# Optimization experiments

Hardware: AMD Instinct MI355X
Metric: run time of the kernel (lower is better)

Reference implementation:

```python
import jax, jax.numpy as jnp
import numpy as np

N_HEAD = 12
N_EMBD = 768


def setup_inputs() -> dict:
    key = jax.random.key(0)
    ks = jax.random.split(key, 5)
    B, T, C = 8, 1024, N_EMBD
    x = jax.random.normal(ks[0], (B, T, C), dtype=jnp.float32)
    # c_attn: Linear(C, 3C); c_proj: Linear(C, C). PyTorch Linear: y = x @ W.T + b
    s = 1.0 / np.sqrt(C)
    W_attn = jax.random.uniform(ks[1], (3 * C, C), minval=-s, maxval=s, dtype=jnp.float32)
    b_attn = jax.random.uniform(ks[2], (3 * C,), minval=-s, maxval=s, dtype=jnp.float32)
    W_proj = jax.random.uniform(ks[3], (C, C), minval=-s, maxval=s, dtype=jnp.float32)
    b_proj = jax.random.uniform(ks[4], (C,), minval=-s, maxval=s, dtype=jnp.float32)
    return {"x": x, "W_attn": W_attn, "b_attn": b_attn, "W_proj": W_proj, "b_proj": b_proj}


def reference(x, W_attn, b_attn, W_proj, b_proj):
    B, T, C = x.shape
    H = N_HEAD
    hs = C // H  # head size
    qkv = x @ W_attn.T + b_attn  # [B, T, 3C]
    q, k, v = jnp.split(qkv, 3, axis=2)
    # [B, T, H, hs] -> [B, H, T, hs]
    q = q.reshape(B, T, H, hs).transpose(0, 2, 1, 3)
    k = k.reshape(B, T, H, hs).transpose(0, 2, 1, 3)
    v = v.reshape(B, T, H, hs).transpose(0, 2, 1, 3)
    att = jnp.einsum('bhqd,bhkd->bhqk', q, k) * (1.0 / np.sqrt(hs))
    causal = jnp.tril(jnp.ones((T, T), dtype=bool))
    att = jnp.where(causal, att, -jnp.inf)
    att = jax.nn.softmax(att, axis=-1)
    y = jnp.einsum('bhqk,bhkd->bhqd', att, v)  # [B, H, T, hs]
    y = y.transpose(0, 2, 1, 3).reshape(B, T, C)
    return y @ W_proj.T + b_proj
```

## Files before the change

### kernel.cpp

```cpp
#include <hip/hip_runtime.h>

typedef unsigned short u16;
typedef unsigned int u32;
typedef __attribute__((ext_vector_type(8))) __bf16 bf16x8;
typedef __attribute__((ext_vector_type(4))) float f32x4;
typedef __attribute__((ext_vector_type(4))) int i32x4;

#define MFMA16(a, b, c) __builtin_amdgcn_mfma_f32_16x16x32_bf16(a, b, c, 0, 0, 0)

__device__ __forceinline__ u16 f2b(float f) {
  __bf16 h = (__bf16)f;
  return __builtin_bit_cast(u16, h);
}

__device__ __forceinline__ void gl_lds16(const void* g, void* l) {
  __builtin_amdgcn_global_load_lds(
      (const __attribute__((address_space(1))) void*)g,
      (__attribute__((address_space(3))) void*)l, 16, 0, 0);
}

__device__ __forceinline__ bf16x8 ldf(const void* p) {
  return __builtin_bit_cast(bf16x8, *(const i32x4*)p);
}

__global__ __launch_bounds__(256) void cvt3_kernel(
    const float4* __restrict__ a, ushort4* __restrict__ oa, int na4,
    const float4* __restrict__ b, ushort4* __restrict__ ob, int nb4,
    const float4* __restrict__ c, ushort4* __restrict__ oc, int nc4) {
  const int step = gridDim.x * blockDim.x;
  const int t0 = blockIdx.x * blockDim.x + threadIdx.x;
  for (int i = t0; i < na4; i += step) {
    float4 v = a[i];
    ushort4 o; o.x = f2b(v.x); o.y = f2b(v.y); o.z = f2b(v.z); o.w = f2b(v.w);
    oa[i] = o;
  }
  for (int i = t0; i < nb4; i += step) {
    float4 v = b[i];
    ushort4 o; o.x = f2b(v.x); o.y = f2b(v.y); o.z = f2b(v.z); o.w = f2b(v.w);
    ob[i] = o;
  }
  for (int i = t0; i < nc4; i += step) {
    float4 v = c[i];
    ushort4 o; o.x = f2b(v.x); o.y = f2b(v.y); o.z = f2b(v.z); o.w = f2b(v.w);
    oc[i] = o;
  }
}

template <int BM, int EPI>
__global__ __launch_bounds__(256, 3) void gemm4(
    const u16* __restrict__ A, const u16* __restrict__ B,
    const float* __restrict__ bias, int M, int N, int K,
    u16* __restrict__ q_s, u16* __restrict__ k_s, u16* __restrict__ vt_s,
    float* __restrict__ outf) {
  constexpr int BN = 192;
  constexpr int MR = BM / 32;
  constexpr int NR = 6;
  constexpr int IA = BM / 32;
  constexpr int IB = 6;
  __shared__ __align__(16) u16 As[BM * 64];
  __shared__ __align__(16) u16 Bs[BN * 64];
  const int tid = threadIdx.x;
  const int w = tid >> 6, l = tid & 63;
  const int lo = l & 15, hi = l >> 4;
  const int wr = w >> 1, wc = w & 1;
  const int nwg = gridDim.x * gridDim.y;
  int bid = blockIdx.y * gridDim.x + blockIdx.x;
  bid = (bid & 7) * (nwg >> 3) + (bid >> 3);
  const int bm0 = (bid / gridDim.x) * BM;
  const int bn0 = (bid % gridDim.x) * BN;
  const size_t Kb = (size_t)K * 2;
  const char* Ab = (const char*)A;
  const char* Bb = (const char*)B;
  const int lrow8 = l >> 3;
  const int lcol = (l & 7) * 16;

  f32x4 acc[MR][NR] = {};

  for (int kt = 0; kt < K; kt += 64) {
    __syncthreads();
#pragma unroll
    for (int i = 0; i < IA; ++i) {
      int rl = (w * IA + i) * 8 + lrow8;
      int cb = lcol ^ ((rl & 7) << 4);
      gl_lds16(Ab + (size_t)(bm0 + rl) * Kb + kt * 2 + cb,
               (char*)As + (w * IA + i) * 1024);
    }
#pragma unroll
    for (int i = 0; i < IB; ++i) {
      int rl = (w * IB + i) * 8 + lrow8;
      int cb = lcol ^ ((rl & 7) << 4);
      gl_lds16(Bb + (size_t)(bn0 + rl) * Kb + kt * 2 + cb,
               (char*)Bs + (w * IB + i) * 1024);
    }
    __syncthreads();
#pragma unroll
    for (int ks = 0; ks < 2; ++ks) {
      bf16x8 bfr[NR];
#pragma unroll
      for (int nf = 0; nf < NR; ++nf) {
        int r = wc * 96 + nf * 16 + lo;
        bfr[nf] = ldf((char*)Bs + r * 128 + ((ks * 64 + hi * 16) ^ ((r & 7) << 4)));
      }
#pragma unroll
      for (int mf = 0; mf < MR; ++mf) {
        int r = wr * (MR * 16) + mf * 16 + lo;
        bf16x8 afr = ldf((char*)As + r * 128 + ((ks * 64 + hi * 16) ^ ((r & 7) << 4)));
#pragma unroll
        for (int nf = 0; nf < NR; ++nf) acc[mf][nf] = MFMA16(afr, bfr[nf], acc[mf][nf]);
      }
    }
  }

#pragma unroll
  for (int nf = 0; nf < NR; ++nf) {
    int col = bn0 + wc * 96 + nf * 16 + lo;
    float bv = bias[col];
    if (EPI == 0) {
      int seg = col / 768;
      int cs = col - seg * 768;
      int h = cs >> 6, d = cs & 63;
      u16* dst = (seg == 0) ? q_s : k_s;
#pragma unroll
      for (int mf = 0; mf < MR; ++mf) {
        int m0 = bm0 + wr * (MR * 16) + mf * 16 + hi * 4;
        int bb = m0 >> 10, t0 = m0 & 1023;
        size_t bh = (size_t)(bb * 12 + h);
        if (seg < 2) {
#pragma unroll
          for (int r = 0; r < 4; ++r)
            dst[(bh * 1024 + t0 + r) * 64 + d] = f2b(acc[mf][nf][r] + bv);
        } else {
          ushort4 pk;
          pk.x = f2b(acc[mf][nf][0] + bv);
          pk.y = f2b(acc[mf][nf][1] + bv);
          pk.z = f2b(acc[mf][nf][2] + bv);
          pk.w = f2b(acc[mf][nf][3] + bv);
          *(ushort4*)&vt_s[(bh * 64 + d) * 1024 + t0] = pk;
        }
      }
    } else {
#pragma unroll
      for (int mf = 0; mf < MR; ++mf) {
        int m0 = bm0 + wr * (MR * 16) + mf * 16 + hi * 4;
#pragma unroll
        for (int r = 0; r < 4; ++r) outf[(size_t)(m0 + r) * N + col] = acc[mf][nf][r] + bv;
      }
    }
  }
}

__global__ __launch_bounds__(256) void attn_kernel(
    const u16* __restrict__ Q, const u16* __restrict__ Kg,
    const u16* __restrict__ Vt, u16* __restrict__ Y) {
  __shared__ __align__(16) u16 Ks[3][64 * 64];
  __shared__ __align__(16) u16 Vs[3][64 * 64];
  const int tid = threadIdx.x;
  const int w = tid >> 6, l = tid & 63;
  const int lo = l & 15, hi = l >> 4;
  int bid = blockIdx.y * gridDim.x + blockIdx.x;
  bid = (bid & 7) * 96 + (bid >> 3);
  const int bh = bid >> 3;
  const int pr = bid & 7;
  const int b = bh / 12, h = bh % 12;
  const float c1 = 0.125f * 1.44269504f;
  const int swl = (lo & 7) << 4;
  const u16* Qb = Q + (size_t)bh * 65536;
  const char* Kbp = (const char*)(Kg + (size_t)bh * 65536);
  const char* Vbp = (const char*)(Vt + (size_t)bh * 65536);
  const int shbase = lo + ((l & 16) ? 32 : 0);
  const bool hiLow = (l & 32) == 0;

  bf16x8 onesv;
#pragma unroll
  for (int j = 0; j < 8; ++j) onesv[j] = (__bf16)1.0f;

  auto STAGE = [&](int buf, int kb) {
#pragma unroll
    for (int i = 0; i < 2; ++i) {
      int c = w * 2 + i;
      int row = c * 8 + (l >> 3);
      int cb = ((l & 7) * 16) ^ ((row & 7) << 4);
      gl_lds16(Kbp + (size_t)(kb + row) * 128 + cb, (char*)&Ks[buf][0] + c * 1024);
      gl_lds16(Vbp + (size_t)row * 2048 + (size_t)kb * 2 + cb, (char*)&Vs[buf][0] + c * 1024);
    }
  };

  for (int sg = 0; sg < 2; ++sg) {
    const int tile = sg ? (15 - pr) : pr;
    const int q0 = tile * 64 + w * 16;
    const int nt = tile + 1;
    const int qr = q0 + lo;

    bf16x8 qf[2];
#pragma unroll
    for (int ks = 0; ks < 2; ++ks)
      qf[ks] = ldf(Qb + (size_t)(q0 + lo) * 64 + ks * 32 + hi * 8);

    f32x4 o[4] = {};
    f32x4 lsum = {0.f, 0.f, 0.f, 0.f};
    float mrow = -1e30f;

    __builtin_amdgcn_s_barrier();
    STAGE(0, 0);
    if (nt > 1) STAGE(1, 64);

    for (int kt = 0; kt < nt; ++kt) {
      if (kt + 1 < nt)
        asm volatile("s_waitcnt vmcnt(4)" ::: "memory");
      else
        asm volatile("s_waitcnt vmcnt(0)" ::: "memory");
      __builtin_amdgcn_s_barrier();
      __builtin_amdgcn_sched_barrier(0);
      if (kt + 2 < nt) STAGE((kt + 2) % 3, (kt + 2) * 64);
      const char* Kt = (const char*)&Ks[kt % 3][0];
      const char* Vv = (const char*)&Vs[kt % 3][0];
      const int kb = kt * 64;

      f32x4 st[4] = {};
      __builtin_amdgcn_s_setprio(1);
#pragma unroll
      for (int kf = 0; kf < 4; ++kf) {
        int rb = (kf * 16 + lo) * 128;
#pragma unroll
        for (int ks = 0; ks < 2; ++ks)
          st[kf] = MFMA16(ldf(Kt + rb + ((ks * 64 + hi * 16) ^ swl)), qf[ks], st[kf]);
      }
      __builtin_amdgcn_s_setprio(0);
      bf16x8 vb[4][2];
#pragma unroll
      for (int nd = 0; nd < 4; ++nd) {
        int rb = (nd * 16 + lo) * 128;
#pragma unroll
        for (int ks = 0; ks < 2; ++ks)
          vb[nd][ks] = ldf(Vv + rb + ((ks * 64 + hi * 16) ^ swl));
      }
      if (kt == nt - 1) {
#pragma unroll
        for (int kf = 0; kf < 4; ++kf)
#pragma unroll
          for (int r = 0; r < 4; ++r) {
            int kcol = kb + kf * 16 + hi * 4 + r;
            if (kcol > qr) st[kf][r] = -1e30f;
          }
      }
      float lm = st[0][0];
#pragma unroll
      for (int kf = 0; kf < 4; ++kf)
#pragma unroll
        for (int r = 0; r < 4; ++r) lm = fmaxf(lm, st[kf][r]);
      lm = fmaxf(lm, __shfl_xor(lm, 16));
      lm = fmaxf(lm, __shfl_xor(lm, 32));
      if (__any(lm * c1 > mrow + 8.0f)) {
        float Mn = fmaxf(mrow, lm * c1);
        float alP = __builtin_amdgcn_exp2f(mrow - Mn);
        mrow = Mn;
        f32x4 alo;
#pragma unroll
        for (int r = 0; r < 4; ++r) alo[r] = __shfl(alP, hi * 4 + r);
#pragma unroll
        for (int nd = 0; nd < 4; ++nd)
#pragma unroll
          for (int r = 0; r < 4; ++r) o[nd][r] *= alo[r];
#pragma unroll
        for (int r = 0; r < 4; ++r) lsum[r] *= alo[r];
      }
#pragma unroll
      for (int kf = 0; kf < 4; ++kf)
#pragma unroll
        for (int r = 0; r < 4; ++r)
          st[kf][r] = __builtin_amdgcn_exp2f(fmaf(st[kf][r], c1, -mrow));
      u32 pk[4][2];
#pragma unroll
      for (int kf = 0; kf < 4; ++kf)
#pragma unroll
        for (int rp = 0; rp < 2; ++rp)
          pk[kf][rp] = (u32)f2b(st[kf][2 * rp]) | ((u32)f2b(st[kf][2 * rp + 1]) << 16);
      bf16x8 pa[2];
#pragma unroll
      for (int ks = 0; ks < 2; ++ks) {
        i32x4 wv;
#pragma unroll
        for (int s = 0; s < 4; ++s) {
          int src = shbase + ((s >> 1) << 4);
          u32 xa = __shfl(pk[2 * ks][s & 1], src);
          u32 xb = __shfl(pk[2 * ks + 1][s & 1], src);
          wv[s] = (int)(hiLow ? xa : xb);
        }
        pa[ks] = __builtin_bit_cast(bf16x8, wv);
      }
      __builtin_amdgcn_s_setprio(1);
#pragma unroll
      for (int ks = 0; ks < 2; ++ks) {
#pragma unroll
        for (int nd = 0; nd < 4; ++nd) o[nd] = MFMA16(pa[ks], vb[nd][ks], o[nd]);
        lsum = MFMA16(pa[ks], onesv, lsum);
      }
      __builtin_amdgcn_s_setprio(0);
    }

    f32x4 inv;
#pragma unroll
    for (int r = 0; r < 4; ++r) inv[r] = 1.0f / lsum[r];
#pragma unroll
    for (int nd = 0; nd < 4; ++nd)
#pragma unroll
      for (int r = 0; r < 4; ++r) {
        int t = q0 + hi * 4 + r;
        int d = nd * 16 + lo;
        Y[((size_t)b * 1024 + t) * 768 + h * 64 + d] = f2b(o[nd][r] * inv[r]);
      }
  }
}

extern "C" void kernel_launch(void* const* d_in, const int* in_sizes, int n_in,
                              void* d_out, int out_size, void* d_ws, size_t ws_size,
                              hipStream_t stream) {
  const float* x  = (const float*)d_in[0];
  const float* Wa = (const float*)d_in[1];
  const float* ba = (const float*)d_in[2];
  const float* Wp = (const float*)d_in[3];
  const float* bp = (const float*)d_in[4];
  float* out = (float*)d_out;
  char* ws = (char*)d_ws;

  constexpr size_t XB  = 0;
  constexpr size_t WAB = 12582912;
  constexpr size_t WPB = WAB + 3538944;
  constexpr size_t QS  = WPB + 1179648;
  constexpr size_t KS  = QS + 12582912;
  constexpr size_t VTS = KS + 12582912;
  constexpr size_t YB  = VTS + 12582912;

  u16* xb  = (u16*)(ws + XB);
  u16* wab = (u16*)(ws + WAB);
  u16* wpb = (u16*)(ws + WPB);
  u16* qs  = (u16*)(ws + QS);
  u16* ks  = (u16*)(ws + KS);
  u16* vts = (u16*)(ws + VTS);
  u16* yb  = (u16*)(ws + YB);

  cvt3_kernel<<<2048, 256, 0, stream>>>(
      (const float4*)x,  (ushort4*)xb,  8192 * 768 / 4,
      (const float4*)Wa, (ushort4*)wab, 2304 * 768 / 4,
      (const float4*)Wp, (ushort4*)wpb, 768 * 768 / 4);

  gemm4<128, 0><<<dim3(12, 64), 256, 0, stream>>>(xb, wab, ba, 8192, 2304, 768,
                                                  qs, ks, vts, nullptr);
  attn_kernel<<<dim3(8, 96), 256, 0, stream>>>(qs, ks, vts, yb);
  gemm4<64, 1><<<dim3(4, 128), 256, 0, stream>>>(yb, wpb, bp, 8192, 768, 768,
                                                 nullptr, nullptr, nullptr, out);
}
```

Measured before the change: 113.8 us.

## Use double-buffered K/V staging and an LDS round-trip for the P transpose

Reduces the K/V LDS ring from three buffers to two and issues the next tile's load at the top of each iteration, adding a trailing barrier per iteration to protect buffer reuse. Replaces the 16 cross-lane shuffles that rearranged bf16 P into MFMA A-operand layout with a per-wave LDS write and swizzled read. The row-max shuffle reduction now runs only inside the rescale branch. Trades less prefetch depth and an extra barrier for cheaper P layout conversion and lower LDS use, which may raise occupancy.

```diff
diff --git a/kernel.cpp b/kernel.cpp
--- a/kernel.cpp
+++ b/kernel.cpp
@@ -2,6 +2,7 @@
 
 typedef unsigned short u16;
 typedef unsigned int u32;
+typedef unsigned long long u64;
 typedef __attribute__((ext_vector_type(8))) __bf16 bf16x8;
 typedef __attribute__((ext_vector_type(4))) float f32x4;
 typedef __attribute__((ext_vector_type(4))) int i32x4;
@@ -152,8 +153,9 @@
 __global__ __launch_bounds__(256) void attn_kernel(
     const u16* __restrict__ Q, const u16* __restrict__ Kg,
     const u16* __restrict__ Vt, u16* __restrict__ Y) {
-  __shared__ __align__(16) u16 Ks[3][64 * 64];
-  __shared__ __align__(16) u16 Vs[3][64 * 64];
+  __shared__ __align__(16) u16 Ks[2][64 * 64];
+  __shared__ __align__(16) u16 Vs[2][64 * 64];
+  __shared__ __align__(16) u16 Ps[4][16 * 64];
   const int tid = threadIdx.x;
   const int w = tid >> 6, l = tid & 63;
   const int lo = l & 15, hi = l >> 4;
@@ -163,12 +165,11 @@
   const int pr = bid & 7;
   const int b = bh / 12, h = bh % 12;
   const float c1 = 0.125f * 1.44269504f;
+  char* pw = (char*)&Ps[w][0];
   const int swl = (lo & 7) << 4;
   const u16* Qb = Q + (size_t)bh * 65536;
   const char* Kbp = (const char*)(Kg + (size_t)bh * 65536);
   const char* Vbp = (const char*)(Vt + (size_t)bh * 65536);
-  const int shbase = lo + ((l & 16) ? 32 : 0);
-  const bool hiLow = (l & 32) == 0;
 
   bf16x8 onesv;
 #pragma unroll
@@ -200,20 +201,19 @@
     f32x4 lsum = {0.f, 0.f, 0.f, 0.f};
     float mrow = -1e30f;
 
-    __builtin_amdgcn_s_barrier();
     STAGE(0, 0);
-    if (nt > 1) STAGE(1, 64);
-
     for (int kt = 0; kt < nt; ++kt) {
-      if (kt + 1 < nt)
+      const int cur = kt & 1;
+      if (kt + 1 < nt) {
+        STAGE(cur ^ 1, (kt + 1) * 64);
         asm volatile("s_waitcnt vmcnt(4)" ::: "memory");
-      else
+      } else {
         asm volatile("s_waitcnt vmcnt(0)" ::: "memory");
+      }
       __builtin_amdgcn_s_barrier();
       __builtin_amdgcn_sched_barrier(0);
-      if (kt + 2 < nt) STAGE((kt + 2) % 3, (kt + 2) * 64);
-      const char* Kt = (const char*)&Ks[kt % 3][0];
-      const char* Vv = (const char*)&Vs[kt % 3][0];
+      const char* Kt = (const char*)&Ks[cur][0];
+      const char* Vv = (const char*)&Vs[cur][0];
       const int kb = kt * 64;
 
       f32x4 st[4] = {};
@@ -248,10 +248,10 @@
       for (int kf = 0; kf < 4; ++kf)
 #pragma unroll
         for (int r = 0; r < 4; ++r) lm = fmaxf(lm, st[kf][r]);
-      lm = fmaxf(lm, __shfl_xor(lm, 16));
-      lm = fmaxf(lm, __shfl_xor(lm, 32));
       if (__any(lm * c1 > mrow + 8.0f)) {
-        float Mn = fmaxf(mrow, lm * c1);
+        float LM = fmaxf(lm, __shfl_xor(lm, 16));
+        LM = fmaxf(LM, __shfl_xor(LM, 32));
+        float Mn = fmaxf(mrow, LM * c1);
         float alP = __builtin_amdgcn_exp2f(mrow - Mn);
         mrow = Mn;
         f32x4 alo;
@@ -269,25 +269,17 @@
 #pragma unroll
         for (int r = 0; r < 4; ++r)
           st[kf][r] = __builtin_amdgcn_exp2f(fmaf(st[kf][r], c1, -mrow));
-      u32 pk[4][2];
-#pragma unroll
-      for (int kf = 0; kf < 4; ++kf)
-#pragma unroll
-        for (int rp = 0; rp < 2; ++rp)
-          pk[kf][rp] = (u32)f2b(st[kf][2 * rp]) | ((u32)f2b(st[kf][2 * rp + 1]) << 16);
+#pragma unroll
+      for (int kf = 0; kf < 4; ++kf) {
+        u32 w0 = (u32)f2b(st[kf][0]) | ((u32)f2b(st[kf][1]) << 16);
+        u32 w1 = (u32)f2b(st[kf][2]) | ((u32)f2b(st[kf][3]) << 16);
+        *(u64*)(pw + lo * 128 + ((kf * 32 + hi * 8) ^ swl)) =
+            (u64)w0 | ((u64)w1 << 32);
+      }
       bf16x8 pa[2];
 #pragma unroll
-      for (int ks = 0; ks < 2; ++ks) {
-        i32x4 wv;
-#pragma unroll
-        for (int s = 0; s < 4; ++s) {
-          int src = shbase + ((s >> 1) << 4);
-          u32 xa = __shfl(pk[2 * ks][s & 1], src);
-          u32 xb = __shfl(pk[2 * ks + 1][s & 1], src);
-          wv[s] = (int)(hiLow ? xa : xb);
-        }
-        pa[ks] = __builtin_bit_cast(bf16x8, wv);
-      }
+      for (int ks = 0; ks < 2; ++ks)
+        pa[ks] = ldf(pw + lo * 128 + ((ks * 64 + hi * 16) ^ swl));
       __builtin_amdgcn_s_setprio(1);
 #pragma unroll
       for (int ks = 0; ks < 2; ++ks) {
@@ -296,6 +288,8 @@
         lsum = MFMA16(pa[ks], onesv, lsum);
       }
       __builtin_amdgcn_s_setprio(0);
+      __builtin_amdgcn_sched_barrier(0);
+      __builtin_amdgcn_s_barrier();
     }
 
     f32x4 inv;
```

Measured after the change: 96.44 us. 1.18x faster.
